# Kernel optimization log

Hardware: AMD Instinct MI355X
Metric: run time of the kernel (lower is better)

The kernel has to match this reference:

```python
import jax, jax.numpy as jnp
import numpy as np

N = 100000   # nodes
E = 800000   # directed edges
IN = 256     # in_channels (== hidden, required by repo's vn MLP dims)
HID = 256    # hidden_channels
OUT = 40     # out_channels (arxiv classes)
EPS = 1e-5


def setup_inputs() -> dict:
    key = jax.random.key(0)
    ks = jax.random.split(key, 8)
    def nrm(k, shape, scale=0.05):
        return jax.random.normal(k, shape, dtype=jnp.float32) * scale
    return {
        "x": nrm(ks[0], (N, IN), 1.0),
        "edge_index": jax.random.randint(ks[1], (2, E), 0, N, dtype=jnp.int32),
        # GCNConv weights (PyG: x @ W, then normalized aggregation, then + bias)
        "W0": nrm(ks[2], (IN, HID)),  "b0": jnp.zeros((HID,), jnp.float32),
        "W1": nrm(ks[3], (HID, HID)), "b1": jnp.zeros((HID,), jnp.float32),
        "W2": nrm(ks[4], (HID, OUT)), "b2": jnp.zeros((OUT,), jnp.float32),
        # BatchNorm1d affine params (batch-stat math, training mode)
        "bn_g0": jnp.ones((HID,), jnp.float32), "bn_b0": jnp.zeros((HID,), jnp.float32),
        "bn_g1": jnp.ones((HID,), jnp.float32), "bn_b1": jnp.zeros((HID,), jnp.float32),
        # virtual node embedding (init to 0 per reset_parameters)
        "vn_emb": jnp.zeros((1, IN), jnp.float32),
        # mlp_vns[0]: Linear(IN,HID) + LayerNorm(HID) + ReLU
        "vn_W0": nrm(ks[5], (IN, HID)),  "vn_b0": jnp.zeros((HID,), jnp.float32),
        "ln_g0": jnp.ones((HID,), jnp.float32), "ln_b0": jnp.zeros((HID,), jnp.float32),
        # mlp_vns[1]: Linear(HID,HID) + LayerNorm(HID) + ReLU
        "vn_W1": nrm(ks[6], (HID, HID)), "vn_b1": jnp.zeros((HID,), jnp.float32),
        "ln_g1": jnp.ones((HID,), jnp.float32), "ln_b1": jnp.zeros((HID,), jnp.float32),
    }


def _forward(x, edge_index, W0, b0, W1, b1, W2, b2, bn_g0, bn_b0, bn_g1, bn_b1,
             vn_emb, vn_W0, vn_b0, ln_g0, ln_b0, vn_W1, vn_b1, ln_g1, ln_b1):
    src, dst = edge_index[0], edge_index[1]
    # GCN symmetric normalization with self-loops: deg = in-degree + 1
    deg = jax.ops.segment_sum(jnp.ones(src.shape, jnp.float32), dst, num_segments=N) + 1.0
    dis = jax.lax.rsqrt(deg)                       # deg^{-1/2}  [N]
    coef = (dis[src] * dis[dst])[:, None]          # edge norm   [E,1]
    self_coef = (dis * dis)[:, None]               # self-loop norm = deg^{-1}  [N,1]

    def gcn(h, W, b):
        h = h @ W                                             # [N, out]
        agg = jax.ops.segment_sum(h[src] * coef, dst, num_segments=N)
        return agg + h * self_coef + b

    def bn(h, g, bv):  # BatchNorm1d, batch statistics over nodes
        mu = h.mean(0)
        var = ((h - mu) ** 2).mean(0)
        return (h - mu) * jax.lax.rsqrt(var + EPS) * g + bv

    def ln(h, g, bv):  # LayerNorm over last dim
        mu = h.mean(-1, keepdims=True)
        var = ((h - mu) ** 2).mean(-1, keepdims=True)
        return (h - mu) * jax.lax.rsqrt(var + EPS) * g + bv

    vx = vn_emb                                   # [1, IN]
    # layer 0
    h = x + vx                                    # virtual-node broadcast
    h = gcn(h, W0, b0)
    h = jax.nn.relu(bn(h, bn_g0, bn_b0))          # dropout = identity (eval)
    pool = jnp.sum(h, axis=0, keepdims=True)      # global_add_pool
    vx = jax.nn.relu(ln((pool + vx) @ vn_W0 + vn_b0, ln_g0, ln_b0))
    # layer 1
    h = h + vx
    h = gcn(h, W1, b1)
    h = jax.nn.relu(bn(h, bn_g1, bn_b1))
    pool = jnp.sum(h, axis=0, keepdims=True)
    vx = jax.nn.relu(ln((pool + vx) @ vn_W1 + vn_b1, ln_g1, ln_b1))
    # layer 2 (output)
    h = h + vx
    h = gcn(h, W2, b2)
    return jax.nn.log_softmax(h, axis=-1)


def reference(x, edge_index, W0, b0, W1, b1, W2, b2, bn_g0, bn_b0, bn_g1, bn_b1,
              vn_emb, vn_W0, vn_b0, ln_g0, ln_b0, vn_W1, vn_b1, ln_g1, ln_b1):
    return _forward(x, edge_index, W0, b0, W1, b1, W2, b2, bn_g0, bn_b0, bn_g1, bn_b1,
                    vn_emb, vn_W0, vn_b0, ln_g0, ln_b0, vn_W1, vn_b1, ln_g1, ln_b1)
```

## Files before the change

kernel.cpp:

```cpp
#include <hip/hip_runtime.h>
#include <hip/hip_bf16.h>
#include <cstdint>

#define N_NODES 100000
#define N_EDGES 800000
#define CH      256
#define COUT    40
#define COUTP   48
#define EPS     1e-5f
#define SCAN_CHUNK 1024
#define NSCAN_BLK  98
#define SB_NBLK 500
#define SB_ROWS 200
#define AGG_NPW 16

typedef unsigned short u16;
typedef unsigned int   u32;
typedef short s16x8 __attribute__((ext_vector_type(8)));
typedef float f32x4 __attribute__((ext_vector_type(4)));

__device__ __forceinline__ float b2f(u32 u) { return __uint_as_float(u << 16); }
__device__ __forceinline__ u16 f2b(float f) {
    u32 u = __float_as_uint(f);
    u32 r = (u + 0x7fffu + ((u >> 16) & 1u)) >> 16;
    return (u16)r;
}
__device__ __forceinline__ u32 packb(float a, float b) {
    return (u32)f2b(a) | ((u32)f2b(b) << 16);
}
__device__ __forceinline__ void unpack8(uint4 v, float* f) {
    f[0] = b2f(v.x & 0xffffu); f[1] = b2f(v.x >> 16);
    f[2] = b2f(v.y & 0xffffu); f[3] = b2f(v.y >> 16);
    f[4] = b2f(v.z & 0xffffu); f[5] = b2f(v.z >> 16);
    f[6] = b2f(v.w & 0xffffu); f[7] = b2f(v.w >> 16);
}

__global__ void k_count(const int* __restrict__ dst, int* __restrict__ counts) {
    int e = blockIdx.x * 256 + threadIdx.x;
    if (e < N_EDGES) atomicAdd(&counts[dst[e]], 1);
}

__global__ void k_scan1(const int* __restrict__ counts, int* __restrict__ partial,
                        int* __restrict__ blocksums) {
    __shared__ int sdata[256];
    int base = blockIdx.x * SCAN_CHUNK;
    int t = threadIdx.x;
    int v[4]; int s = 0;
    for (int j = 0; j < 4; j++) {
        int i = base + t * 4 + j;
        v[j] = (i < N_NODES) ? counts[i] : 0;
        s += v[j];
    }
    sdata[t] = s; __syncthreads();
    for (int off = 1; off < 256; off <<= 1) {
        int x = (t >= off) ? sdata[t - off] : 0;
        __syncthreads();
        sdata[t] += x;
        __syncthreads();
    }
    int incl = sdata[t];
    int run = incl - s;
    if (t == 255) blocksums[blockIdx.x] = incl;
    for (int j = 0; j < 4; j++) {
        int i = base + t * 4 + j;
        if (i < N_NODES) partial[i] = run;
        run += v[j];
    }
}

__global__ void k_scan2(int* __restrict__ blocksums) {
    __shared__ int sd[128];
    int t = threadIdx.x;
    int v = (t < NSCAN_BLK) ? blocksums[t] : 0;
    sd[t] = v; __syncthreads();
    for (int off = 1; off < 128; off <<= 1) {
        int x = (t >= off) ? sd[t - off] : 0;
        __syncthreads();
        sd[t] += x;
        __syncthreads();
    }
    if (t < NSCAN_BLK) blocksums[t] = sd[t] - v;
}

__global__ void k_scan3(int* __restrict__ row_start, const int* __restrict__ blocksums,
                        int* __restrict__ cursor) {
    int i = blockIdx.x * 256 + threadIdx.x;
    if (i < N_NODES) {
        int v = row_start[i] + blocksums[i >> 10];
        row_start[i] = v;
        cursor[i] = v;
    }
}

__global__ void k_dis(const int* __restrict__ counts, float* __restrict__ dis) {
    int i = blockIdx.x * 256 + threadIdx.x;
    if (i < N_NODES) dis[i] = rsqrtf(1.0f + (float)counts[i]);
}

__global__ void k_fill(const int* __restrict__ src, const int* __restrict__ dst,
                       int* __restrict__ cursor, int* __restrict__ csr,
                       const float* __restrict__ dis, float* __restrict__ coefv) {
    int e = blockIdx.x * 256 + threadIdx.x;
    if (e < N_EDGES) {
        int d = dst[e], s = src[e];
        int p = atomicAdd(&cursor[d], 1);
        csr[p] = s;
        coefv[p] = dis[s] * dis[d];
    }
}

__global__ void k_wt(const float* __restrict__ W, u16* __restrict__ Wt, int ncols) {
    int n = blockIdx.x, k = threadIdx.x;
    float v = (n < ncols) ? W[k * ncols + n] : 0.f;
    Wt[n * 256 + k] = f2b(v);
}

__global__ void k_xconv(const float* __restrict__ x, u16* __restrict__ xb) {
    int idx = (blockIdx.x * 256 + threadIdx.x) * 8;
    float4 a = *(const float4*)(x + idx);
    float4 b = *(const float4*)(x + idx + 4);
    uint4 o = {packb(a.x, a.y), packb(a.z, a.w), packb(b.x, b.y), packb(b.z, b.w)};
    *(uint4*)(xb + idx) = o;
}

__global__ void k_vecmat(const float* __restrict__ vec, const float* __restrict__ W,
                         int ncols, int npad, float* __restrict__ outv) {
    __shared__ float s[256];
    int t = threadIdx.x;
    s[t] = vec[t];
    __syncthreads();
    float acc = 0.f;
    if (t < ncols) {
        for (int k = 0; k < 256; k++) acc += s[k] * W[k * ncols + t];
    }
    if (t < npad) outv[t] = acc;
}

__global__ __launch_bounds__(256) void k_gemm(const u16* __restrict__ A,
                                              const u16* __restrict__ Wt,
                                              u16* __restrict__ Hout) {
    __shared__ u16 Bs[256 * 40];
    const int t = threadIdx.x;
    const int wave = t >> 6, lane = t & 63;
    const int lm = lane & 15, quad = lane >> 4;
    const int m0 = blockIdx.x * 64;
    const f32x4 vz = {0.f, 0.f, 0.f, 0.f};
    f32x4 acc[4][4];
    for (int m = 0; m < 4; m++)
        for (int c = 0; c < 4; c++) acc[m][c] = vz;

    for (int k0 = 0; k0 < 256; k0 += 32) {
        {
            const uint4* srcp = (const uint4*)(Wt + t * 256 + k0);
            uint4* dl = (uint4*)(Bs + t * 40);
            dl[0] = srcp[0]; dl[1] = srcp[1]; dl[2] = srcp[2]; dl[3] = srcp[3];
        }
        __syncthreads();
        s16x8 afrag[4];
#pragma unroll
        for (int m = 0; m < 4; m++) {
            int row = m0 + m * 16 + lm;
            if (row < N_NODES) afrag[m] = *(const s16x8*)(A + (size_t)row * 256 + k0 + quad * 8);
            else { s16x8 z = {0,0,0,0,0,0,0,0}; afrag[m] = z; }
        }
#pragma unroll
        for (int c = 0; c < 4; c++) {
            s16x8 bfrag = *(const s16x8*)(Bs + (wave * 64 + c * 16 + lm) * 40 + quad * 8);
#pragma unroll
            for (int m = 0; m < 4; m++)
                acc[m][c] = __builtin_amdgcn_mfma_f32_16x16x32_bf16(afrag[m], bfrag, acc[m][c], 0, 0, 0);
        }
        __syncthreads();
    }
#pragma unroll
    for (int m = 0; m < 4; m++) {
#pragma unroll
        for (int c = 0; c < 4; c++) {
            int col = wave * 64 + c * 16 + lm;
#pragma unroll
            for (int i = 0; i < 4; i++) {
                int row = m0 + m * 16 + quad * 4 + i;
                if (row < N_NODES) Hout[(size_t)row * 256 + col] = f2b(acc[m][c][i]);
            }
        }
    }
}

__global__ __launch_bounds__(256) void k_gemm2(const u16* __restrict__ A,
                                               const u16* __restrict__ Wt,
                                               u16* __restrict__ Hout) {
    __shared__ u16 Bs[48 * 40];
    const int t = threadIdx.x;
    const int wave = t >> 6, lane = t & 63;
    const int lm = lane & 15, quad = lane >> 4;
    const int m0 = blockIdx.x * 64;
    const f32x4 vz = {0.f, 0.f, 0.f, 0.f};
    f32x4 acc[3]; acc[0] = vz; acc[1] = vz; acc[2] = vz;

    for (int k0 = 0; k0 < 256; k0 += 32) {
        if (t < 48) {
            const uint4* srcp = (const uint4*)(Wt + t * 256 + k0);
            uint4* dl = (uint4*)(Bs + t * 40);
            dl[0] = srcp[0]; dl[1] = srcp[1]; dl[2] = srcp[2]; dl[3] = srcp[3];
        }
        __syncthreads();
        int row = m0 + wave * 16 + lm;
        s16x8 af;
        if (row < N_NODES) af = *(const s16x8*)(A + (size_t)row * 256 + k0 + quad * 8);
        else { s16x8 z = {0,0,0,0,0,0,0,0}; af = z; }
#pragma unroll
        for (int c = 0; c < 3; c++) {
            s16x8 bf = *(const s16x8*)(Bs + (c * 16 + lm) * 40 + quad * 8);
            acc[c] = __builtin_amdgcn_mfma_f32_16x16x32_bf16(af, bf, acc[c], 0, 0, 0);
        }
        __syncthreads();
    }
#pragma unroll
    for (int c = 0; c < 3; c++) {
        int col = c * 16 + lm;
#pragma unroll
        for (int i = 0; i < 4; i++) {
            int row = m0 + wave * 16 + quad * 4 + i;
            if (row < N_NODES) Hout[(size_t)row * COUTP + col] = f2b(acc[c][i]);
        }
    }
}

__global__ __launch_bounds__(256) void k_agg(const u16* __restrict__ H2,
                                             const int* __restrict__ row_start,
                                             const int* __restrict__ counts,
                                             const int* __restrict__ csr,
                                             const float* __restrict__ coefv,
                                             const float* __restrict__ dis,
                                             const float* __restrict__ bias,
                                             const float* __restrict__ v2,
                                             u16* __restrict__ OutB,
                                             float* __restrict__ stats) {
    __shared__ float ls[512];
    const int t = threadIdx.x, wave = t >> 6, lane = t & 63, ci = lane * 4;
    const float4 bb = *(const float4*)(bias + ci);
    const float4 vv = *(const float4*)(v2 + ci);
    float s0=0,s1=0,s2=0,s3=0,q0=0,q1=0,q2=0,q3=0;
    const int nbase = blockIdx.x * (4 * AGG_NPW) + wave * AGG_NPW;
    for (int i = 0; i < AGG_NPW; i++) {
        const int node = nbase + i;
        if (node >= N_NODES) break;
        const int beg = row_start[node], cnt = counts[node];
        const float dn = dis[node];
        float a0=0,a1=0,a2=0,a3=0, cs=0;
        int e = 0;
        for (; e + 4 <= cnt; e += 4) {
            int ia = csr[beg+e], ib = csr[beg+e+1], ic = csr[beg+e+2], id = csr[beg+e+3];
            float ca = coefv[beg+e], cb = coefv[beg+e+1], cc = coefv[beg+e+2], cd = coefv[beg+e+3];
            uint2 ra = *(const uint2*)(H2 + (size_t)ia * 256 + ci);
            uint2 rb = *(const uint2*)(H2 + (size_t)ib * 256 + ci);
            uint2 rc = *(const uint2*)(H2 + (size_t)ic * 256 + ci);
            uint2 rd = *(const uint2*)(H2 + (size_t)id * 256 + ci);
            cs += ca + cb + cc + cd;
            a0 += ca*b2f(ra.x&0xffffu) + cb*b2f(rb.x&0xffffu) + cc*b2f(rc.x&0xffffu) + cd*b2f(rd.x&0xffffu);
            a1 += ca*b2f(ra.x>>16)     + cb*b2f(rb.x>>16)     + cc*b2f(rc.x>>16)     + cd*b2f(rd.x>>16);
            a2 += ca*b2f(ra.y&0xffffu) + cb*b2f(rb.y&0xffffu) + cc*b2f(rc.y&0xffffu) + cd*b2f(rd.y&0xffffu);
            a3 += ca*b2f(ra.y>>16)     + cb*b2f(rb.y>>16)     + cc*b2f(rc.y>>16)     + cd*b2f(rd.y>>16);
        }
        for (; e < cnt; e++) {
            int ia = csr[beg+e]; float ca = coefv[beg+e];
            uint2 ra = *(const uint2*)(H2 + (size_t)ia * 256 + ci);
            cs += ca;
            a0 += ca*b2f(ra.x&0xffffu); a1 += ca*b2f(ra.x>>16);
            a2 += ca*b2f(ra.y&0xffffu); a3 += ca*b2f(ra.y>>16);
        }
        uint2 rs = *(const uint2*)(H2 + (size_t)node * 256 + ci);
        const float sc = dn * dn, cv = cs + sc;
        float f0 = a0 + sc*b2f(rs.x&0xffffu) + cv*vv.x + bb.x;
        float f1 = a1 + sc*b2f(rs.x>>16)     + cv*vv.y + bb.y;
        float f2 = a2 + sc*b2f(rs.y&0xffffu) + cv*vv.z + bb.z;
        float f3 = a3 + sc*b2f(rs.y>>16)     + cv*vv.w + bb.w;
        uint2 o; o.x = packb(f0, f1); o.y = packb(f2, f3);
        *(uint2*)(OutB + (size_t)node * 256 + ci) = o;
        s0 += f0; q0 += f0*f0; s1 += f1; q1 += f1*f1;
        s2 += f2; q2 += f2*f2; s3 += f3; q3 += f3*f3;
    }
    ls[t] = 0.f; ls[256 + t] = 0.f;
    __syncthreads();
    atomicAdd(&ls[ci], s0);   atomicAdd(&ls[ci+1], s1);
    atomicAdd(&ls[ci+2], s2); atomicAdd(&ls[ci+3], s3);
    atomicAdd(&ls[256+ci], q0);   atomicAdd(&ls[256+ci+1], q1);
    atomicAdd(&ls[256+ci+2], q2); atomicAdd(&ls[256+ci+3], q3);
    __syncthreads();
    atomicAdd(&stats[t], ls[t]);
    atomicAdd(&stats[256 + t], ls[256 + t]);
}

__global__ void k_fin(const float* __restrict__ stats, const float* __restrict__ g,
                      const float* __restrict__ bb, float* __restrict__ ggbc) {
    int t = threadIdx.x;
    const float inv = 1.0f / (float)N_NODES;
    float mu = stats[t] * inv;
    float var = stats[256 + t] * inv - mu * mu;
    float rs = rsqrtf(var + EPS);
    float gg = g[t] * rs;
    ggbc[t] = gg;
    ggbc[256 + t] = bb[t] - mu * gg;
}

__global__ __launch_bounds__(256) void k_bnrelu(const u16* __restrict__ OutB,
                                                const float* __restrict__ ggbc,
                                                u16* __restrict__ Hr,
                                                float* __restrict__ pool) {
    __shared__ float lp[256];
    const int t = threadIdx.x;
    const int cg = (t & 31) * 8;
    const int rg = t >> 5;
    const int r0 = blockIdx.x * SB_ROWS + rg;
    float gg[8], bc[8];
    {
        float4 a = *(const float4*)(ggbc + cg);
        float4 b = *(const float4*)(ggbc + cg + 4);
        float4 c = *(const float4*)(ggbc + 256 + cg);
        float4 d = *(const float4*)(ggbc + 256 + cg + 4);
        gg[0]=a.x; gg[1]=a.y; gg[2]=a.z; gg[3]=a.w; gg[4]=b.x; gg[5]=b.y; gg[6]=b.z; gg[7]=b.w;
        bc[0]=c.x; bc[1]=c.y; bc[2]=c.z; bc[3]=c.w; bc[4]=d.x; bc[5]=d.y; bc[6]=d.z; bc[7]=d.w;
    }
    float ps[8];
#pragma unroll
    for (int j = 0; j < 8; j++) ps[j] = 0.f;
#pragma unroll 2
    for (int it = 0; it < SB_ROWS / 8; it++) {
        int r = r0 + it * 8;
        uint4 v = *(const uint4*)(OutB + (size_t)r * 256 + cg);
        float f[8]; unpack8(v, f);
#pragma unroll
        for (int j = 0; j < 8; j++) {
            f[j] = fmaxf(f[j] * gg[j] + bc[j], 0.f);
            ps[j] += f[j];
        }
        uint4 o = {packb(f[0], f[1]), packb(f[2], f[3]), packb(f[4], f[5]), packb(f[6], f[7])};
        *(uint4*)(Hr + (size_t)r * 256 + cg) = o;
    }
    lp[t] = 0.f;
    __syncthreads();
#pragma unroll
    for (int j = 0; j < 8; j++) atomicAdd(&lp[cg + j], ps[j]);
    __syncthreads();
    atomicAdd(&pool[t], lp[t]);
}

__global__ void k_vx(const float* __restrict__ pool, const float* __restrict__ vx_old,
                     const float* __restrict__ vnW, const float* __restrict__ vnb,
                     const float* __restrict__ lng, const float* __restrict__ lnb,
                     float* __restrict__ vx_new,
                     const float* __restrict__ Wnext, int ncn, int npn,
                     float* __restrict__ v2n) {
    __shared__ float s[256];
    __shared__ float red[256];
    int t = threadIdx.x;
    s[t] = pool[t] + vx_old[t];
    __syncthreads();
    float y = vnb[t];
    for (int k = 0; k < 256; k++) y += s[k] * vnW[k * 256 + t];
    red[t] = y; __syncthreads();
    for (int off = 128; off > 0; off >>= 1) {
        if (t < off) red[t] += red[t + off];
        __syncthreads();
    }
    float mu = red[0] * (1.f / 256.f);
    __syncthreads();
    float d = y - mu;
    red[t] = d * d; __syncthreads();
    for (int off = 128; off > 0; off >>= 1) {
        if (t < off) red[t] += red[t + off];
        __syncthreads();
    }
    float var = red[0] * (1.f / 256.f);
    float v = fmaxf(d * rsqrtf(var + EPS) * lng[t] + lnb[t], 0.f);
    vx_new[t] = v;
    __syncthreads();
    s[t] = v;
    __syncthreads();
    float acc = 0.f;
    if (t < ncn) {
        for (int k = 0; k < 256; k++) acc += s[k] * Wnext[k * ncn + t];
    }
    if (t < npn) v2n[t] = acc;
}

__global__ __launch_bounds__(256) void k_agg2(const u16* __restrict__ H2,
                                              const int* __restrict__ row_start,
                                              const int* __restrict__ counts,
                                              const int* __restrict__ csr,
                                              const float* __restrict__ coefv,
                                              const float* __restrict__ dis,
                                              const float* __restrict__ bias,
                                              const float* __restrict__ v2,
                                              float* __restrict__ OutF) {
    const int t = threadIdx.x, wave = t >> 6, lane = t & 63;
    const int half = lane >> 5, hl = lane & 31;
    const bool gact = hl < 24;
    const bool cact = hl < 20;
    const int c0 = 2 * hl;
    float bb0 = 0.f, bb1 = 0.f, vv0 = 0.f, vv1 = 0.f;
    if (cact) {
        float2 bv = *(const float2*)(bias + c0); bb0 = bv.x; bb1 = bv.y;
        float2 vvv = *(const float2*)(v2 + c0);  vv0 = vvv.x; vv1 = vvv.y;
    }
    const int nbase = blockIdx.x * 16 + wave * 4;
    for (int i = 0; i < 4; i++) {
        const int node = nbase + i;
        const int beg = row_start[node], cnt = counts[node];
        const float dn = dis[node];
        float a0 = 0.f, a1 = 0.f, cs = 0.f;
        int e = half;
        for (; e + 6 < cnt; e += 8) {
            int ia = csr[beg+e], ib = csr[beg+e+2], ic = csr[beg+e+4], id = csr[beg+e+6];
            float ca = coefv[beg+e], cb = coefv[beg+e+2], cc = coefv[beg+e+4], cd = coefv[beg+e+6];
            u32 ra = 0, rb = 0, rc = 0, rd = 0;
            if (gact) {
                ra = *(const u32*)(H2 + (size_t)ia * COUTP + c0);
                rb = *(const u32*)(H2 + (size_t)ib * COUTP + c0);
                rc = *(const u32*)(H2 + (size_t)ic * COUTP + c0);
                rd = *(const u32*)(H2 + (size_t)id * COUTP + c0);
            }
            cs += ca + cb + cc + cd;
            a0 += ca*b2f(ra&0xffffu) + cb*b2f(rb&0xffffu) + cc*b2f(rc&0xffffu) + cd*b2f(rd&0xffffu);
            a1 += ca*b2f(ra>>16)     + cb*b2f(rb>>16)     + cc*b2f(rc>>16)     + cd*b2f(rd>>16);
        }
        for (; e < cnt; e += 2) {
            int ia = csr[beg+e]; float ca = coefv[beg+e];
            u32 ra = gact ? *(const u32*)(H2 + (size_t)ia * COUTP + c0) : 0u;
            cs += ca;
            a0 += ca*b2f(ra&0xffffu); a1 += ca*b2f(ra>>16);
        }
        a0 += __shfl_xor(a0, 32);
        a1 += __shfl_xor(a1, 32);
        cs += __shfl_xor(cs, 32);
        const float sc = dn * dn;
        u32 rs_ = gact ? *(const u32*)(H2 + (size_t)node * COUTP + c0) : 0u;
        float h0 = a0 + sc*b2f(rs_&0xffffu) + (cs+sc)*vv0 + bb0;
        float h1 = a1 + sc*b2f(rs_>>16)     + (cs+sc)*vv1 + bb1;
        float m = cact ? fmaxf(h0, h1) : -3.0e38f;
#pragma unroll
        for (int off = 16; off > 0; off >>= 1) m = fmaxf(m, __shfl_xor(m, off));
        float ex = cact ? (expf(h0 - m) + expf(h1 - m)) : 0.f;
        float se = ex;
#pragma unroll
        for (int off = 16; off > 0; off >>= 1) se += __shfl_xor(se, off);
        float lg = logf(se);
        if (cact && half == 0) {
            float2 o = {h0 - m - lg, h1 - m - lg};
            *(float2*)(OutF + (size_t)node * COUT + c0) = o;
        }
    }
}

extern "C" void kernel_launch(void* const* d_in, const int* in_sizes, int n_in,
                              void* d_out, int out_size, void* d_ws, size_t ws_size,
                              hipStream_t stream) {
    const float* x   = (const float*)d_in[0];
    const int*   ei  = (const int*)d_in[1];
    const int*   esrc = ei;
    const int*   edst = ei + N_EDGES;
    const float* W0 = (const float*)d_in[2];  const float* b0 = (const float*)d_in[3];
    const float* W1 = (const float*)d_in[4];  const float* b1 = (const float*)d_in[5];
    const float* W2 = (const float*)d_in[6];  const float* b2 = (const float*)d_in[7];
    const float* bg0 = (const float*)d_in[8]; const float* bb0 = (const float*)d_in[9];
    const float* bg1 = (const float*)d_in[10]; const float* bb1 = (const float*)d_in[11];
    const float* vn_emb = (const float*)d_in[12];
    const float* vW0 = (const float*)d_in[13]; const float* vb0 = (const float*)d_in[14];
    const float* lg0 = (const float*)d_in[15]; const float* lb0 = (const float*)d_in[16];
    const float* vW1 = (const float*)d_in[17]; const float* vb1 = (const float*)d_in[18];
    const float* lg1 = (const float*)d_in[19]; const float* lb1 = (const float*)d_in[20];

    char* w = (char*)d_ws;
    auto alloc = [&](size_t bytes) { void* p = (void*)w; w += ((bytes + 255) / 256) * 256; return p; };
    u16* H2    = (u16*)alloc((size_t)N_NODES * 256 * 2);
    u16* HR    = (u16*)alloc((size_t)N_NODES * 256 * 2);
    u16* OutB  = (u16*)alloc((size_t)N_NODES * 256 * 2);
    int* csr   = (int*)alloc((size_t)N_EDGES * 4);
    float* coefv = (float*)alloc((size_t)N_EDGES * 4);
    int* counts = (int*)alloc((size_t)N_NODES * 4);
    int* rowst  = (int*)alloc((size_t)N_NODES * 4);
    int* cursor = (int*)alloc((size_t)N_NODES * 4);
    float* dis  = (float*)alloc((size_t)N_NODES * 4);
    u16* Wtb0 = (u16*)alloc(256 * 256 * 2);
    u16* Wtb1 = (u16*)alloc(256 * 256 * 2);
    u16* Wt2b = (u16*)alloc(COUTP * 256 * 2);
    int* scanblk = (int*)alloc(128 * 4);
    float* stats = (float*)alloc(768 * 4);
    float* ggbc  = (float*)alloc(512 * 4);
    float* vxA = (float*)alloc(256 * 4);
    float* vxB = (float*)alloc(256 * 4);
    float* v20 = (float*)alloc(256 * 4);
    float* v21 = (float*)alloc(256 * 4);
    float* v22 = (float*)alloc(64 * 4);
    (void)ws_size; (void)in_sizes; (void)n_in; (void)out_size; (void)vxB;

    hipMemsetAsync(counts, 0, (size_t)N_NODES * 4, stream);
    k_count<<<(N_EDGES + 255) / 256, 256, 0, stream>>>(edst, counts);
    k_dis<<<(N_NODES + 255) / 256, 256, 0, stream>>>(counts, dis);
    k_scan1<<<NSCAN_BLK, 256, 0, stream>>>(counts, rowst, scanblk);
    k_scan2<<<1, 128, 0, stream>>>(scanblk);
    k_scan3<<<(N_NODES + 255) / 256, 256, 0, stream>>>(rowst, scanblk, cursor);
    k_fill<<<(N_EDGES + 255) / 256, 256, 0, stream>>>(esrc, edst, cursor, csr, dis, coefv);

    k_wt<<<256, 256, 0, stream>>>(W0, Wtb0, 256);
    k_wt<<<256, 256, 0, stream>>>(W1, Wtb1, 256);
    k_wt<<<COUTP, 256, 0, stream>>>(W2, Wt2b, COUT);
    k_xconv<<<(N_NODES * 256 / 8 + 255) / 256, 256, 0, stream>>>(x, HR);
    k_vecmat<<<1, 256, 0, stream>>>(vn_emb, W0, 256, 256, v20);

    const int aggblk = (N_NODES + 63) / 64;

    k_gemm<<<(N_NODES + 63) / 64, 256, 0, stream>>>(HR, Wtb0, H2);
    hipMemsetAsync(stats, 0, 768 * 4, stream);
    k_agg<<<aggblk, 256, 0, stream>>>(H2, rowst, counts, csr, coefv, dis, b0, v20, OutB, stats);
    k_fin<<<1, 256, 0, stream>>>(stats, bg0, bb0, ggbc);
    k_bnrelu<<<SB_NBLK, 256, 0, stream>>>(OutB, ggbc, HR, stats + 512);
    k_vx<<<1, 256, 0, stream>>>(stats + 512, vn_emb, vW0, vb0, lg0, lb0, vxA, W1, 256, 256, v21);

    k_gemm<<<(N_NODES + 63) / 64, 256, 0, stream>>>(HR, Wtb1, H2);
    hipMemsetAsync(stats, 0, 768 * 4, stream);
    k_agg<<<aggblk, 256, 0, stream>>>(H2, rowst, counts, csr, coefv, dis, b1, v21, OutB, stats);
    k_fin<<<1, 256, 0, stream>>>(stats, bg1, bb1, ggbc);
    k_bnrelu<<<SB_NBLK, 256, 0, stream>>>(OutB, ggbc, HR, stats + 512);
    k_vx<<<1, 256, 0, stream>>>(stats + 512, vxA, vW1, vb1, lg1, lb1, vxB, W2, COUT, COUTP, v22);

    k_gemm2<<<(N_NODES + 63) / 64, 256, 0, stream>>>(HR, Wt2b, H2);
    k_agg2<<<N_NODES / 16, 256, 0, stream>>>(H2, rowst, counts, csr, coefv, dis, b2, v22, (float*)d_out);
}
```

Before: 833.0 us.

## Split aggregation into column-slab passes and fuse small setup kernels

The neighbor aggregation is restructured into four passes, each covering a 64-channel slab. Within a pass, 8 lanes handle one node with 16-byte loads, so the gathered slab of H2 (about 12.8MB) is more likely to stay resident in cache across random neighbor reads. The degree computation is folded into scan3, the three weight transposes are merged into one launch, and BN finalization moves into bnrelu, which removes several small launches. The cost is that the CSR indices and coefficients are reread four times and there are more agg launches.

```diff
diff --git a/kernel.cpp b/kernel.cpp
--- a/kernel.cpp
+++ b/kernel.cpp
@@ -12,7 +12,7 @@
 #define NSCAN_BLK  98
 #define SB_NBLK 500
 #define SB_ROWS 200
-#define AGG_NPW 16
+#define NAGG_BLK 782
 
 typedef unsigned short u16;
 typedef unsigned int   u32;
@@ -83,18 +83,15 @@
 }
 
 __global__ void k_scan3(int* __restrict__ row_start, const int* __restrict__ blocksums,
-                        int* __restrict__ cursor) {
+                        int* __restrict__ cursor, const int* __restrict__ counts,
+                        float* __restrict__ dis) {
     int i = blockIdx.x * 256 + threadIdx.x;
     if (i < N_NODES) {
         int v = row_start[i] + blocksums[i >> 10];
         row_start[i] = v;
         cursor[i] = v;
-    }
-}
-
-__global__ void k_dis(const int* __restrict__ counts, float* __restrict__ dis) {
-    int i = blockIdx.x * 256 + threadIdx.x;
-    if (i < N_NODES) dis[i] = rsqrtf(1.0f + (float)counts[i]);
+        dis[i] = rsqrtf(1.0f + (float)counts[i]);
+    }
 }
 
 __global__ void k_fill(const int* __restrict__ src, const int* __restrict__ dst,
@@ -109,10 +106,19 @@
     }
 }
 
-__global__ void k_wt(const float* __restrict__ W, u16* __restrict__ Wt, int ncols) {
-    int n = blockIdx.x, k = threadIdx.x;
-    float v = (n < ncols) ? W[k * ncols + n] : 0.f;
-    Wt[n * 256 + k] = f2b(v);
+__global__ void k_wt3(const float* __restrict__ W0, const float* __restrict__ W1,
+                      const float* __restrict__ W2,
+                      u16* __restrict__ T0, u16* __restrict__ T1, u16* __restrict__ T2) {
+    int b = blockIdx.x, k = threadIdx.x;
+    if (b < 256) {
+        T0[b * 256 + k] = f2b(W0[k * 256 + b]);
+    } else if (b < 512) {
+        int n = b - 256;
+        T1[n * 256 + k] = f2b(W1[k * 256 + n]);
+    } else {
+        int n = b - 512;
+        T2[n * 256 + k] = f2b(n < COUT ? W2[k * COUT + n] : 0.f);
+    }
 }
 
 __global__ void k_xconv(const float* __restrict__ x, u16* __restrict__ xb) {
@@ -235,76 +241,82 @@
                                              const float* __restrict__ bias,
                                              const float* __restrict__ v2,
                                              u16* __restrict__ OutB,
-                                             float* __restrict__ stats) {
-    __shared__ float ls[512];
-    const int t = threadIdx.x, wave = t >> 6, lane = t & 63, ci = lane * 4;
-    const float4 bb = *(const float4*)(bias + ci);
-    const float4 vv = *(const float4*)(v2 + ci);
-    float s0=0,s1=0,s2=0,s3=0,q0=0,q1=0,q2=0,q3=0;
-    const int nbase = blockIdx.x * (4 * AGG_NPW) + wave * AGG_NPW;
-    for (int i = 0; i < AGG_NPW; i++) {
+                                             float* __restrict__ stats,
+                                             int ci0) {
+    __shared__ float ls[128];
+    const int t = threadIdx.x, wave = t >> 6, lane = t & 63;
+    const int grp = lane >> 3, gl = lane & 7;
+    const int ci = ci0 + gl * 8;
+    float bb[8], vv[8];
+    {
+        float4 a = *(const float4*)(bias + ci);
+        float4 b = *(const float4*)(bias + ci + 4);
+        float4 c = *(const float4*)(v2 + ci);
+        float4 d = *(const float4*)(v2 + ci + 4);
+        bb[0]=a.x; bb[1]=a.y; bb[2]=a.z; bb[3]=a.w; bb[4]=b.x; bb[5]=b.y; bb[6]=b.z; bb[7]=b.w;
+        vv[0]=c.x; vv[1]=c.y; vv[2]=c.z; vv[3]=c.w; vv[4]=d.x; vv[5]=d.y; vv[6]=d.z; vv[7]=d.w;
+    }
+    float s[8], q[8];
+#pragma unroll
+    for (int j = 0; j < 8; j++) { s[j] = 0.f; q[j] = 0.f; }
+    const int nbase = blockIdx.x * 128 + wave * 32 + grp * 4;
+    for (int i = 0; i < 4; i++) {
         const int node = nbase + i;
         if (node >= N_NODES) break;
         const int beg = row_start[node], cnt = counts[node];
         const float dn = dis[node];
-        float a0=0,a1=0,a2=0,a3=0, cs=0;
+        float a[8];
+#pragma unroll
+        for (int j = 0; j < 8; j++) a[j] = 0.f;
+        float cs = 0.f;
         int e = 0;
-        for (; e + 4 <= cnt; e += 4) {
-            int ia = csr[beg+e], ib = csr[beg+e+1], ic = csr[beg+e+2], id = csr[beg+e+3];
-            float ca = coefv[beg+e], cb = coefv[beg+e+1], cc = coefv[beg+e+2], cd = coefv[beg+e+3];
-            uint2 ra = *(const uint2*)(H2 + (size_t)ia * 256 + ci);
-            uint2 rb = *(const uint2*)(H2 + (size_t)ib * 256 + ci);
-            uint2 rc = *(const uint2*)(H2 + (size_t)ic * 256 + ci);
-            uint2 rd = *(const uint2*)(H2 + (size_t)id * 256 + ci);
-            cs += ca + cb + cc + cd;
-            a0 += ca*b2f(ra.x&0xffffu) + cb*b2f(rb.x&0xffffu) + cc*b2f(rc.x&0xffffu) + cd*b2f(rd.x&0xffffu);
-            a1 += ca*b2f(ra.x>>16)     + cb*b2f(rb.x>>16)     + cc*b2f(rc.x>>16)     + cd*b2f(rd.x>>16);
-            a2 += ca*b2f(ra.y&0xffffu) + cb*b2f(rb.y&0xffffu) + cc*b2f(rc.y&0xffffu) + cd*b2f(rd.y&0xffffu);
-            a3 += ca*b2f(ra.y>>16)     + cb*b2f(rb.y>>16)     + cc*b2f(rc.y>>16)     + cd*b2f(rd.y>>16);
-        }
-        for (; e < cnt; e++) {
-            int ia = csr[beg+e]; float ca = coefv[beg+e];
-            uint2 ra = *(const uint2*)(H2 + (size_t)ia * 256 + ci);
+        for (; e + 2 <= cnt; e += 2) {
+            int ia = csr[beg + e], ib = csr[beg + e + 1];
+            float ca = coefv[beg + e], cb = coefv[beg + e + 1];
+            uint4 ra = *(const uint4*)(H2 + (size_t)ia * 256 + ci);
+            uint4 rb = *(const uint4*)(H2 + (size_t)ib * 256 + ci);
+            cs += ca + cb;
+            float fa[8], fb[8]; unpack8(ra, fa); unpack8(rb, fb);
+#pragma unroll
+            for (int j = 0; j < 8; j++) a[j] += ca * fa[j] + cb * fb[j];
+        }
+        if (e < cnt) {
+            int ia = csr[beg + e]; float ca = coefv[beg + e];
+            uint4 ra = *(const uint4*)(H2 + (size_t)ia * 256 + ci);
             cs += ca;
-            a0 += ca*b2f(ra.x&0xffffu); a1 += ca*b2f(ra.x>>16);
-            a2 += ca*b2f(ra.y&0xffffu); a3 += ca*b2f(ra.y>>16);
-        }
-        uint2 rs = *(const uint2*)(H2 + (size_t)node * 256 + ci);
+            float fa[8]; unpack8(ra, fa);
+#pragma unroll
+            for (int j = 0; j < 8; j++) a[j] += ca * fa[j];
+        }
+        uint4 rs = *(const uint4*)(H2 + (size_t)node * 256 + ci);
+        float fs[8]; unpack8(rs, fs);
         const float sc = dn * dn, cv = cs + sc;
-        float f0 = a0 + sc*b2f(rs.x&0xffffu) + cv*vv.x + bb.x;
-        float f1 = a1 + sc*b2f(rs.x>>16)     + cv*vv.y + bb.y;
-        float f2 = a2 + sc*b2f(rs.y&0xffffu) + cv*vv.z + bb.z;
-        float f3 = a3 + sc*b2f(rs.y>>16)     + cv*vv.w + bb.w;
-        uint2 o; o.x = packb(f0, f1); o.y = packb(f2, f3);
-        *(uint2*)(OutB + (size_t)node * 256 + ci) = o;
-        s0 += f0; q0 += f0*f0; s1 += f1; q1 += f1*f1;
-        s2 += f2; q2 += f2*f2; s3 += f3; q3 += f3*f3;
-    }
-    ls[t] = 0.f; ls[256 + t] = 0.f;
-    __syncthreads();
-    atomicAdd(&ls[ci], s0);   atomicAdd(&ls[ci+1], s1);
-    atomicAdd(&ls[ci+2], s2); atomicAdd(&ls[ci+3], s3);
-    atomicAdd(&ls[256+ci], q0);   atomicAdd(&ls[256+ci+1], q1);
-    atomicAdd(&ls[256+ci+2], q2); atomicAdd(&ls[256+ci+3], q3);
-    __syncthreads();
-    atomicAdd(&stats[t], ls[t]);
-    atomicAdd(&stats[256 + t], ls[256 + t]);
-}
-
-__global__ void k_fin(const float* __restrict__ stats, const float* __restrict__ g,
-                      const float* __restrict__ bb, float* __restrict__ ggbc) {
-    int t = threadIdx.x;
-    const float inv = 1.0f / (float)N_NODES;
-    float mu = stats[t] * inv;
-    float var = stats[256 + t] * inv - mu * mu;
-    float rs = rsqrtf(var + EPS);
-    float gg = g[t] * rs;
-    ggbc[t] = gg;
-    ggbc[256 + t] = bb[t] - mu * gg;
+        float f[8];
+#pragma unroll
+        for (int j = 0; j < 8; j++) {
+            f[j] = a[j] + sc * fs[j] + cv * vv[j] + bb[j];
+            s[j] += f[j]; q[j] += f[j] * f[j];
+        }
+        uint4 o = {packb(f[0], f[1]), packb(f[2], f[3]), packb(f[4], f[5]), packb(f[6], f[7])};
+        *(uint4*)(OutB + (size_t)node * 256 + ci) = o;
+    }
+    if (t < 128) ls[t] = 0.f;
+    __syncthreads();
+    const int li = gl * 8;
+#pragma unroll
+    for (int j = 0; j < 8; j++) {
+        atomicAdd(&ls[li + j], s[j]);
+        atomicAdd(&ls[64 + li + j], q[j]);
+    }
+    __syncthreads();
+    if (t < 64) atomicAdd(&stats[ci0 + t], ls[t]);
+    else if (t < 128) atomicAdd(&stats[256 + ci0 + (t - 64)], ls[t]);
 }
 
 __global__ __launch_bounds__(256) void k_bnrelu(const u16* __restrict__ OutB,
-                                                const float* __restrict__ ggbc,
+                                                const float* __restrict__ stats,
+                                                const float* __restrict__ g,
+                                                const float* __restrict__ bb_,
                                                 u16* __restrict__ Hr,
                                                 float* __restrict__ pool) {
     __shared__ float lp[256];
@@ -312,14 +324,16 @@
     const int cg = (t & 31) * 8;
     const int rg = t >> 5;
     const int r0 = blockIdx.x * SB_ROWS + rg;
+    const float inv = 1.0f / (float)N_NODES;
     float gg[8], bc[8];
-    {
-        float4 a = *(const float4*)(ggbc + cg);
-        float4 b = *(const float4*)(ggbc + cg + 4);
-        float4 c = *(const float4*)(ggbc + 256 + cg);
-        float4 d = *(const float4*)(ggbc + 256 + cg + 4);
-        gg[0]=a.x; gg[1]=a.y; gg[2]=a.z; gg[3]=a.w; gg[4]=b.x; gg[5]=b.y; gg[6]=b.z; gg[7]=b.w;
-        bc[0]=c.x; bc[1]=c.y; bc[2]=c.z; bc[3]=c.w; bc[4]=d.x; bc[5]=d.y; bc[6]=d.z; bc[7]=d.w;
+#pragma unroll
+    for (int j = 0; j < 8; j++) {
+        int c = cg + j;
+        float mu = stats[c] * inv;
+        float var = stats[256 + c] * inv - mu * mu;
+        float rs = rsqrtf(var + EPS);
+        gg[j] = g[c] * rs;
+        bc[j] = bb_[c] - mu * gg[j];
     }
     float ps[8];
 #pragma unroll
@@ -486,7 +500,6 @@
     u16* Wt2b = (u16*)alloc(COUTP * 256 * 2);
     int* scanblk = (int*)alloc(128 * 4);
     float* stats = (float*)alloc(768 * 4);
-    float* ggbc  = (float*)alloc(512 * 4);
     float* vxA = (float*)alloc(256 * 4);
     float* vxB = (float*)alloc(256 * 4);
     float* v20 = (float*)alloc(256 * 4);
@@ -496,32 +509,27 @@
 
     hipMemsetAsync(counts, 0, (size_t)N_NODES * 4, stream);
     k_count<<<(N_EDGES + 255) / 256, 256, 0, stream>>>(edst, counts);
-    k_dis<<<(N_NODES + 255) / 256, 256, 0, stream>>>(counts, dis);
     k_scan1<<<NSCAN_BLK, 256, 0, stream>>>(counts, rowst, scanblk);
     k_scan2<<<1, 128, 0, stream>>>(scanblk);
-    k_scan3<<<(N_NODES + 255) / 256, 256, 0, stream>>>(rowst, scanblk, cursor);
+    k_scan3<<<(N_NODES + 255) / 256, 256, 0, stream>>>(rowst, scanblk, cursor, counts, dis);
     k_fill<<<(N_EDGES + 255) / 256, 256, 0, stream>>>(esrc, edst, cursor, csr, dis, coefv);
 
-    k_wt<<<256, 256, 0, stream>>>(W0, Wtb0, 256);
-    k_wt<<<256, 256, 0, stream>>>(W1, Wtb1, 256);
-    k_wt<<<COUTP, 256, 0, stream>>>(W2, Wt2b, COUT);
+    k_wt3<<<512 + COUTP, 256, 0, stream>>>(W0, W1, W2, Wtb0, Wtb1, Wt2b);
     k_xconv<<<(N_NODES * 256 / 8 + 255) / 256, 256, 0, stream>>>(x, HR);
     k_vecmat<<<1, 256, 0, stream>>>(vn_emb, W0, 256, 256, v20);
 
-    const int aggblk = (N_NODES + 63) / 64;
-
     k_gemm<<<(N_NODES + 63) / 64, 256, 0, stream>>>(HR, Wtb0, H2);
     hipMemsetAsync(stats, 0, 768 * 4, stream);
-    k_agg<<<aggblk, 256, 0, stream>>>(H2, rowst, counts, csr, coefv, dis, b0, v20, OutB, stats);
-    k_fin<<<1, 256, 0, stream>>>(stats, bg0, bb0, ggbc);
-    k_bnrelu<<<SB_NBLK, 256, 0, stream>>>(OutB, ggbc, HR, stats + 512);
+    for (int p = 0; p < 4; p++)
+        k_agg<<<NAGG_BLK, 256, 0, stream>>>(H2, rowst, counts, csr, coefv, dis, b0, v20, OutB, stats, p * 64);
+    k_bnrelu<<<SB_NBLK, 256, 0, stream>>>(OutB, stats, bg0, bb0, HR, stats + 512);
     k_vx<<<1, 256, 0, stream>>>(stats + 512, vn_emb, vW0, vb0, lg0, lb0, vxA, W1, 256, 256, v21);
 
     k_gemm<<<(N_NODES + 63) / 64, 256, 0, stream>>>(HR, Wtb1, H2);
     hipMemsetAsync(stats, 0, 768 * 4, stream);
-    k_agg<<<aggblk, 256, 0, stream>>>(H2, rowst, counts, csr, coefv, dis, b1, v21, OutB, stats);
-    k_fin<<<1, 256, 0, stream>>>(stats, bg1, bb1, ggbc);
-    k_bnrelu<<<SB_NBLK, 256, 0, stream>>>(OutB, ggbc, HR, stats + 512);
+    for (int p = 0; p < 4; p++)
+        k_agg<<<NAGG_BLK, 256, 0, stream>>>(H2, rowst, counts, csr, coefv, dis, b1, v21, OutB, stats, p * 64);
+    k_bnrelu<<<SB_NBLK, 256, 0, stream>>>(OutB, stats, bg1, bb1, HR, stats + 512);
     k_vx<<<1, 256, 0, stream>>>(stats + 512, vxA, vW1, vb1, lg1, lb1, vxB, W2, COUT, COUTP, v22);
 
     k_gemm2<<<(N_NODES + 63) / 64, 256, 0, stream>>>(HR, Wt2b, H2);
```

Result: slower. 0.9998 ms (+20.0%).
